# Performance work log

Measured on AMD Instinct MI355X. Metric: run time of the kernel, lower is better.

Reference implementation:

```python
import jax, jax.numpy as jnp
import numpy as np

A1, A2 = 16, 16            # block tile sizes (arr_size1, arr_size2)
G = 1000                   # graph_size (max node index + 1)
EG = 16000                 # number of graph edges (avg degree 16)
SIZE1 = G * A1             # input feature length  (16000)
SIZE2 = G * A2             # output feature length (16000)
NNZ = EG * A1 * A2         # expanded COO entries  (4,096,000)
B = 32                     # batch


def _expand_indices(t0, t1, a1, a2):
    """Vectorized adjust_indices: edge (t0,t1) -> tile of (row,col) pairs.
    row = t0*a2 + j, col = t1*a1 + i  for all i in [a1), j in [a2)."""
    e = t0.shape[0]
    j = np.arange(a2)
    i = np.arange(a1)
    rows = np.broadcast_to(t0[:, None, None] * a2 + j[None, None, :], (e, a1, a2)).reshape(-1)
    cols = np.broadcast_to(t1[:, None, None] * a1 + i[None, :, None], (e, a1, a2)).reshape(-1)
    return rows.astype(np.int32), cols.astype(np.int32)


def setup_inputs() -> dict:
    key = jax.random.key(0)
    ks = jax.random.split(key, 6)
    rng = np.random.default_rng(0)
    t0 = rng.integers(0, G, EG)
    t1 = rng.integers(0, G, EG)
    rows_np, cols_np = _expand_indices(t0, t1, A1, A2)
    # original init: uniform(-1/len(indices), 1/len(indices)) with len([2,nnz])==2 -> U(-0.5, 0.5)
    return {
        "x": jax.random.normal(ks[0], (B, SIZE1, 1), dtype=jnp.float32),
        "weight_mean": jax.random.uniform(ks[1], (NNZ,), jnp.float32, -0.5, 0.5),
        "weight_log_var": jnp.zeros((NNZ,), jnp.float32),
        "b_mean": jax.random.uniform(ks[2], (SIZE2,), jnp.float32, -0.5, 0.5),
        "b_log_var": jnp.zeros((SIZE2,), jnp.float32),
        "eps_w": jax.random.normal(ks[3], (NNZ,), dtype=jnp.float32),
        "eps_b": jax.random.normal(ks[4], (SIZE2,), dtype=jnp.float32),
        "rows": jnp.asarray(rows_np),
        "cols": jnp.asarray(cols_np),
    }


def reference(x, weight_mean, weight_log_var, b_mean, b_log_var, eps_w, eps_b, rows, cols):
    # reparameterization sample of sparse weight values
    values = eps_w * jnp.exp(weight_log_var) + weight_mean          # [NNZ]
    # COO spmm: out[b, r, k] += values[e] * x[b, c, k] for each (r, c) = (rows[e], cols[e])
    contrib = values[None, :, None] * x[:, cols, :]                 # [B, NNZ, 1]
    out = jnp.zeros((x.shape[0], SIZE2, x.shape[2]), x.dtype).at[:, rows, :].add(contrib)
    # reparameterized bias, broadcast over batch
    b = eps_b * jnp.exp(b_log_var) + b_mean                         # [SIZE2]
    out = out + b[None, :, None]
    # kl is explicitly zeroed in the source right before return
    return (out, jnp.asarray(0.0, dtype=x.dtype))
```

## Files before the change

kernel.cpp:

```cpp
#include <hip/hip_runtime.h>

#define EG   16000
#define NG   1000
#define BB   32
#define SIZE 16000
#define CAP  64

typedef float f32x4 __attribute__((ext_vector_type(4)));

__global__ __launch_bounds__(256) void pack_kernel(
    const int* __restrict__ rows, const int* __restrict__ cols,
    int* __restrict__ pk)
{
    int e = blockIdx.x * 256 + threadIdx.x;
    if (e < EG) {
        int t0 = rows[(long)e << 8] >> 4;
        int t1 = cols[(long)e << 8] >> 4;
        pk[e] = (t0 << 10) | t1;
    }
}

__global__ __launch_bounds__(256, 4) void spmm_kernel(
    const float* __restrict__ wm, const float* __restrict__ wlv,
    const float* __restrict__ ew, const float* __restrict__ x,
    const float* __restrict__ bm, const float* __restrict__ blv,
    const float* __restrict__ eb, const int* __restrict__ pk,
    float* __restrict__ out)
{
    __shared__ f32x4 vt[2][4][64];
    __shared__ f32x4 xs[2][4][160];
    __shared__ int   sl[CAP];
    __shared__ int   scnt;

    int g   = blockIdx.x;
    int tid = threadIdx.x;

    if (tid == 0) scnt = 0;
    __syncthreads();
    const int4* pk4 = (const int4*)pk;
    for (int c = tid; c < EG / 4; c += 256) {
        int4 v = pk4[c];
        int e0 = c << 2;
        if ((v.x >> 10) == g) { int p = atomicAdd(&scnt, 1); if (p < CAP) sl[p] = ((e0    ) << 10) | (v.x & 1023); }
        if ((v.y >> 10) == g) { int p = atomicAdd(&scnt, 1); if (p < CAP) sl[p] = ((e0 + 1) << 10) | (v.y & 1023); }
        if ((v.z >> 10) == g) { int p = atomicAdd(&scnt, 1); if (p < CAP) sl[p] = ((e0 + 2) << 10) | (v.z & 1023); }
        if ((v.w >> 10) == g) { int p = atomicAdd(&scnt, 1); if (p < CAP) sl[p] = ((e0 + 3) << 10) | (v.w & 1023); }
    }
    __syncthreads();
    int n = scnt; n = n < CAP ? n : CAP;

    int wave = tid >> 6;
    int lane = tid & 63;
    int jg   = lane & 3;
    int cb2  = lane >> 2;

    f32x4 acc0 = {0.f,0.f,0.f,0.f}, acc1 = {0.f,0.f,0.f,0.f};
    f32x4 m4, l4, g4, xv0, xv1;
    int iters = (n + 3) >> 2;
    bool vcur = false, vnxt = false;

    auto issue = [&](int idx) -> bool {
        bool val = idx < n;
        if (val) {
            int pkv = sl[idx];
            int e   = pkv >> 10;
            int t1  = pkv & 1023;
            long wq = ((long)e << 6) + lane;
            m4 = ((const f32x4*)wm)[wq];
            l4 = ((const f32x4*)wlv)[wq];
            g4 = ((const f32x4*)ew)[wq];
            const f32x4* x4 = (const f32x4*)x;
            int c0 = lane, c1 = lane + 64;
            xv0 = x4[(long)(c0 >> 2) * (SIZE/4) + (t1 << 2) + (c0 & 3)];
            xv1 = x4[(long)(c1 >> 2) * (SIZE/4) + (t1 << 2) + (c1 & 3)];
        }
        return val;
    };
    auto writeb = [&](int buf, bool val) {
        if (val) {
            f32x4 v;
            v.x = g4.x * __expf(l4.x) + m4.x;
            v.y = g4.y * __expf(l4.y) + m4.y;
            v.z = g4.z * __expf(l4.z) + m4.z;
            v.w = g4.w * __expf(l4.w) + m4.w;
            vt[buf][wave][lane] = v;
            int c0 = lane, c1 = lane + 64;
            xs[buf][wave][(c0 >> 2) * 5 + (c0 & 3)] = xv0;
            xs[buf][wave][(c1 >> 2) * 5 + (c1 & 3)] = xv1;
        }
    };
    auto compute = [&](int buf, bool val) {
        if (!val) return;
        f32x4 a0 = xs[buf][wave][ cb2       * 5 + 0];
        f32x4 a1 = xs[buf][wave][ cb2       * 5 + 1];
        f32x4 a2 = xs[buf][wave][ cb2       * 5 + 2];
        f32x4 a3 = xs[buf][wave][ cb2       * 5 + 3];
        f32x4 b0 = xs[buf][wave][(cb2 + 16) * 5 + 0];
        f32x4 b1 = xs[buf][wave][(cb2 + 16) * 5 + 1];
        f32x4 b2 = xs[buf][wave][(cb2 + 16) * 5 + 2];
        f32x4 b3 = xs[buf][wave][(cb2 + 16) * 5 + 3];
        float xra[16] = {a0.x,a0.y,a0.z,a0.w, a1.x,a1.y,a1.z,a1.w,
                         a2.x,a2.y,a2.z,a2.w, a3.x,a3.y,a3.z,a3.w};
        float xrb[16] = {b0.x,b0.y,b0.z,b0.w, b1.x,b1.y,b1.z,b1.w,
                         b2.x,b2.y,b2.z,b2.w, b3.x,b3.y,b3.z,b3.w};
        #pragma unroll
        for (int i = 0; i < 16; ++i) {
            f32x4 w = vt[buf][wave][(i << 2) + jg];
            acc0 += w * xra[i];
            acc1 += w * xrb[i];
        }
    };

    vcur = issue(wave);
    writeb(0, vcur);
    __syncthreads();
    for (int it = 0; it < iters; ++it) {
        bool more = (it + 1 < iters);
        if (more) vnxt = issue(((it + 1) << 2) + wave);
        compute(it & 1, vcur);
        if (more) writeb((it + 1) & 1, vnxt);
        __syncthreads();
        vcur = vnxt;
    }

    f32x4* sred = &xs[0][0][0];
    sred[(wave << 7) + (lane << 1) + 0] = acc0;
    sred[(wave << 7) + (lane << 1) + 1] = acc1;
    __syncthreads();
    if (tid < 128) {
        int cb  = tid >> 2;
        int jgf = tid & 3;
        int h   = cb >> 4;
        int sl_ = ((cb & 15) << 2) + jgf;
        f32x4 s = sred[(0 << 7) + (sl_ << 1) + h]
                + sred[(1 << 7) + (sl_ << 1) + h]
                + sred[(2 << 7) + (sl_ << 1) + h]
                + sred[(3 << 7) + (sl_ << 1) + h];
        int r0 = (g << 4) + (jgf << 2);
        f32x4 b4 = *(const f32x4*)&bm[r0];
        f32x4 v4 = *(const f32x4*)&blv[r0];
        f32x4 e4 = *(const f32x4*)&eb[r0];
        f32x4 o;
        o.x = s.x + (e4.x * __expf(v4.x) + b4.x);
        o.y = s.y + (e4.y * __expf(v4.y) + b4.y);
        o.z = s.z + (e4.z * __expf(v4.z) + b4.z);
        o.w = s.w + (e4.w * __expf(v4.w) + b4.w);
        *(f32x4*)&out[(long)cb * SIZE + r0] = o;
    }
    if (g == 0 && tid == 0) out[(long)BB * SIZE] = 0.0f;
}

extern "C" void kernel_launch(void* const* d_in, const int* in_sizes, int n_in,
                              void* d_out, int out_size, void* d_ws, size_t ws_size,
                              hipStream_t stream) {
    const float* x   = (const float*)d_in[0];
    const float* wm  = (const float*)d_in[1];
    const float* wlv = (const float*)d_in[2];
    const float* bm  = (const float*)d_in[3];
    const float* blv = (const float*)d_in[4];
    const float* ew  = (const float*)d_in[5];
    const float* eb  = (const float*)d_in[6];
    const int* rows  = (const int*)d_in[7];
    const int* cols  = (const int*)d_in[8];
    float* out = (float*)d_out;

    int* pk = (int*)d_ws;

    pack_kernel<<<(EG + 255) / 256, 256, 0, stream>>>(rows, cols, pk);
    spmm_kernel<<<NG, 256, 0, stream>>>(wm, wlv, ew, x, bm, blv, eb, pk, out);
}
```

Before: 133.0 us.

## Make staging buffers wave-private and prefetch two edges ahead without block barriers

Each wave now gets its own double-buffered shared-memory region for weights and x tiles, so the per-iteration __syncthreads is replaced by a single barrier before the final reduction. Two register sets (A/B) let each wave issue global loads for the edge two steps ahead while computing the current one, deepening the load pipeline. The inner compute loop is reorganised to read x in f32x4 chunks alongside four weight vectors. The cost is more live registers from the duplicated prefetch state, which may reduce occupancy, and waves with uneven edge counts now run independently.

```diff
diff --git a/kernel.cpp b/kernel.cpp
--- a/kernel.cpp
+++ b/kernel.cpp
@@ -27,8 +27,8 @@
     const float* __restrict__ eb, const int* __restrict__ pk,
     float* __restrict__ out)
 {
-    __shared__ f32x4 vt[2][4][64];
-    __shared__ f32x4 xs[2][4][160];
+    __shared__ f32x4 vt[4][2][64];
+    __shared__ f32x4 xs[4][2][160];
     __shared__ int   sl[CAP];
     __shared__ int   scnt;
 
@@ -39,12 +39,12 @@
     __syncthreads();
     const int4* pk4 = (const int4*)pk;
     for (int c = tid; c < EG / 4; c += 256) {
-        int4 v = pk4[c];
+        int4 w = pk4[c];
         int e0 = c << 2;
-        if ((v.x >> 10) == g) { int p = atomicAdd(&scnt, 1); if (p < CAP) sl[p] = ((e0    ) << 10) | (v.x & 1023); }
-        if ((v.y >> 10) == g) { int p = atomicAdd(&scnt, 1); if (p < CAP) sl[p] = ((e0 + 1) << 10) | (v.y & 1023); }
-        if ((v.z >> 10) == g) { int p = atomicAdd(&scnt, 1); if (p < CAP) sl[p] = ((e0 + 2) << 10) | (v.z & 1023); }
-        if ((v.w >> 10) == g) { int p = atomicAdd(&scnt, 1); if (p < CAP) sl[p] = ((e0 + 3) << 10) | (v.w & 1023); }
+        if ((w.x >> 10) == g) { int p = atomicAdd(&scnt, 1); if (p < CAP) sl[p] = ((e0    ) << 10) | (w.x & 1023); }
+        if ((w.y >> 10) == g) { int p = atomicAdd(&scnt, 1); if (p < CAP) sl[p] = ((e0 + 1) << 10) | (w.y & 1023); }
+        if ((w.z >> 10) == g) { int p = atomicAdd(&scnt, 1); if (p < CAP) sl[p] = ((e0 + 2) << 10) | (w.z & 1023); }
+        if ((w.w >> 10) == g) { int p = atomicAdd(&scnt, 1); if (p < CAP) sl[p] = ((e0 + 3) << 10) | (w.w & 1023); }
     }
     __syncthreads();
     int n = scnt; n = n < CAP ? n : CAP;
@@ -54,75 +54,88 @@
     int jg   = lane & 3;
     int cb2  = lane >> 2;
 
+    int myn = (n > wave) ? (((n - 1 - wave) >> 2) + 1) : 0;
+
     f32x4 acc0 = {0.f,0.f,0.f,0.f}, acc1 = {0.f,0.f,0.f,0.f};
-    f32x4 m4, l4, g4, xv0, xv1;
-    int iters = (n + 3) >> 2;
-    bool vcur = false, vnxt = false;
+    f32x4 mA, lA, gA, x0A, x1A;
+    f32x4 mB, lB, gB, x0B, x1B;
 
-    auto issue = [&](int idx) -> bool {
-        bool val = idx < n;
-        if (val) {
-            int pkv = sl[idx];
-            int e   = pkv >> 10;
-            int t1  = pkv & 1023;
-            long wq = ((long)e << 6) + lane;
-            m4 = ((const f32x4*)wm)[wq];
-            l4 = ((const f32x4*)wlv)[wq];
-            g4 = ((const f32x4*)ew)[wq];
-            const f32x4* x4 = (const f32x4*)x;
-            int c0 = lane, c1 = lane + 64;
-            xv0 = x4[(long)(c0 >> 2) * (SIZE/4) + (t1 << 2) + (c0 & 3)];
-            xv1 = x4[(long)(c1 >> 2) * (SIZE/4) + (t1 << 2) + (c1 & 3)];
-        }
-        return val;
+    auto issueA = [&](int k) {
+        int pkv = sl[wave + (k << 2)];
+        int e   = pkv >> 10, t1 = pkv & 1023;
+        long wq = ((long)e << 6) + lane;
+        mA = ((const f32x4*)wm)[wq];
+        lA = ((const f32x4*)wlv)[wq];
+        gA = ((const f32x4*)ew)[wq];
+        const f32x4* x4 = (const f32x4*)x;
+        int c0 = lane, c1 = lane + 64;
+        x0A = x4[(long)(c0 >> 2) * (SIZE/4) + (t1 << 2) + (c0 & 3)];
+        x1A = x4[(long)(c1 >> 2) * (SIZE/4) + (t1 << 2) + (c1 & 3)];
     };
-    auto writeb = [&](int buf, bool val) {
-        if (val) {
-            f32x4 v;
-            v.x = g4.x * __expf(l4.x) + m4.x;
-            v.y = g4.y * __expf(l4.y) + m4.y;
-            v.z = g4.z * __expf(l4.z) + m4.z;
-            v.w = g4.w * __expf(l4.w) + m4.w;
-            vt[buf][wave][lane] = v;
-            int c0 = lane, c1 = lane + 64;
-            xs[buf][wave][(c0 >> 2) * 5 + (c0 & 3)] = xv0;
-            xs[buf][wave][(c1 >> 2) * 5 + (c1 & 3)] = xv1;
-        }
+    auto issueB = [&](int k) {
+        int pkv = sl[wave + (k << 2)];
+        int e   = pkv >> 10, t1 = pkv & 1023;
+        long wq = ((long)e << 6) + lane;
+        mB = ((const f32x4*)wm)[wq];
+        lB = ((const f32x4*)wlv)[wq];
+        gB = ((const f32x4*)ew)[wq];
+        const f32x4* x4 = (const f32x4*)x;
+        int c0 = lane, c1 = lane + 64;
+        x0B = x4[(long)(c0 >> 2) * (SIZE/4) + (t1 << 2) + (c0 & 3)];
+        x1B = x4[(long)(c1 >> 2) * (SIZE/4) + (t1 << 2) + (c1 & 3)];
     };
-    auto compute = [&](int buf, bool val) {
-        if (!val) return;
-        f32x4 a0 = xs[buf][wave][ cb2       * 5 + 0];
-        f32x4 a1 = xs[buf][wave][ cb2       * 5 + 1];
-        f32x4 a2 = xs[buf][wave][ cb2       * 5 + 2];
-        f32x4 a3 = xs[buf][wave][ cb2       * 5 + 3];
-        f32x4 b0 = xs[buf][wave][(cb2 + 16) * 5 + 0];
-        f32x4 b1 = xs[buf][wave][(cb2 + 16) * 5 + 1];
-        f32x4 b2 = xs[buf][wave][(cb2 + 16) * 5 + 2];
-        f32x4 b3 = xs[buf][wave][(cb2 + 16) * 5 + 3];
-        float xra[16] = {a0.x,a0.y,a0.z,a0.w, a1.x,a1.y,a1.z,a1.w,
-                         a2.x,a2.y,a2.z,a2.w, a3.x,a3.y,a3.z,a3.w};
-        float xrb[16] = {b0.x,b0.y,b0.z,b0.w, b1.x,b1.y,b1.z,b1.w,
-                         b2.x,b2.y,b2.z,b2.w, b3.x,b3.y,b3.z,b3.w};
+    auto writebA = [&](int buf) {
+        f32x4 v;
+        v.x = gA.x * __expf(lA.x) + mA.x;
+        v.y = gA.y * __expf(lA.y) + mA.y;
+        v.z = gA.z * __expf(lA.z) + mA.z;
+        v.w = gA.w * __expf(lA.w) + mA.w;
+        vt[wave][buf][lane] = v;
+        int c0 = lane, c1 = lane + 64;
+        xs[wave][buf][(c0 >> 2) * 5 + (c0 & 3)] = x0A;
+        xs[wave][buf][(c1 >> 2) * 5 + (c1 & 3)] = x1A;
+    };
+    auto writebB = [&](int buf) {
+        f32x4 v;
+        v.x = gB.x * __expf(lB.x) + mB.x;
+        v.y = gB.y * __expf(lB.y) + mB.y;
+        v.z = gB.z * __expf(lB.z) + mB.z;
+        v.w = gB.w * __expf(lB.w) + mB.w;
+        vt[wave][buf][lane] = v;
+        int c0 = lane, c1 = lane + 64;
+        xs[wave][buf][(c0 >> 2) * 5 + (c0 & 3)] = x0B;
+        xs[wave][buf][(c1 >> 2) * 5 + (c1 & 3)] = x1B;
+    };
+    auto compute = [&](int buf) {
         #pragma unroll
-        for (int i = 0; i < 16; ++i) {
-            f32x4 w = vt[buf][wave][(i << 2) + jg];
-            acc0 += w * xra[i];
-            acc1 += w * xrb[i];
+        for (int q = 0; q < 4; ++q) {
+            f32x4 xa = xs[wave][buf][ cb2       * 5 + q];
+            f32x4 xb = xs[wave][buf][(cb2 + 16) * 5 + q];
+            f32x4 w0 = vt[wave][buf][(q << 4) + 0  + jg];
+            f32x4 w1 = vt[wave][buf][(q << 4) + 4  + jg];
+            f32x4 w2 = vt[wave][buf][(q << 4) + 8  + jg];
+            f32x4 w3 = vt[wave][buf][(q << 4) + 12 + jg];
+            acc0 += w0 * xa.x; acc0 += w1 * xa.y;
+            acc0 += w2 * xa.z; acc0 += w3 * xa.w;
+            acc1 += w0 * xb.x; acc1 += w1 * xb.y;
+            acc1 += w2 * xb.z; acc1 += w3 * xb.w;
         }
     };
 
-    vcur = issue(wave);
-    writeb(0, vcur);
-    __syncthreads();
-    for (int it = 0; it < iters; ++it) {
-        bool more = (it + 1 < iters);
-        if (more) vnxt = issue(((it + 1) << 2) + wave);
-        compute(it & 1, vcur);
-        if (more) writeb((it + 1) & 1, vnxt);
-        __syncthreads();
-        vcur = vnxt;
+    if (myn > 0) issueA(0);
+    if (myn > 1) issueB(1);
+    if (myn > 0) writebA(0);
+    for (int k = 0; k < myn; ++k) {
+        compute(k & 1);
+        if (k + 2 < myn) {
+            if ((k & 1) == 0) issueA(k + 2); else issueB(k + 2);
+        }
+        if (k + 1 < myn) {
+            if ((k & 1) == 0) writebB((k + 1) & 1); else writebA((k + 1) & 1);
+        }
     }
 
+    __syncthreads();
     f32x4* sred = &xs[0][0][0];
     sred[(wave << 7) + (lane << 1) + 0] = acc0;
     sred[(wave << 7) + (lane << 1) + 1] = acc1;
```

After: 214.9 us. 61.6% more time.
